# Optimization experiments

Measured on AMD Instinct MI355X. Metric: run time of the kernel, lower is better.

The kernel has to match this reference:

```python
import jax, jax.numpy as jnp
import numpy as np

NUM_LAYERS = 4
D_MODEL = 512
D_INNER = 1024   # 2 * d_model (Mamba expand=2)
D_STATE = 16
DT_RANK = 32     # ceil(d_model / 16)
D_CONV = 4
BATCH = 2
SEQ = 512
EPS = 1e-5


def _rmsnorm(x, w, eps=EPS):
    # fused add+RMSNorm math: fp32 reduction, scale by weight (no bias)
    x = x.astype(jnp.float32)
    return x * jax.lax.rsqrt(jnp.mean(x * x, axis=-1, keepdims=True) + eps) * w


def _silu(x):
    return x * jax.nn.sigmoid(x)


def _causal_conv(x, w, b):
    # x: (B, D, L); w: (D, K) depthwise causal conv, left-pad K-1, take first L
    xp = jnp.pad(x, ((0, 0), (0, 0), (D_CONV - 1, 0)))
    out = jax.lax.conv_general_dilated(
        xp, w[:, None, :], (1,), 'VALID',
        dimension_numbers=('NCH', 'OIH', 'NCH'),
        feature_group_count=x.shape[1])
    return out + b[None, :, None]


def _selective_scan(u, delta, A, Bm, Cm):
    # u, delta: (B, D, L); A: (D, N); Bm, Cm: (B, N, L)
    xs = (jnp.moveaxis(delta, 2, 0), jnp.moveaxis(u, 2, 0),
          jnp.moveaxis(Bm, 2, 0), jnp.moveaxis(Cm, 2, 0))
    h0 = jnp.zeros((u.shape[0], u.shape[1], A.shape[1]), u.dtype)

    def step(h, xst):
        d_t, u_t, b_t, c_t = xst                     # (B,D),(B,D),(B,N),(B,N)
        dA = jnp.exp(d_t[:, :, None] * A[None])      # (B,D,N) ZOH discretization
        h = h * dA + (d_t * u_t)[:, :, None] * b_t[:, None, :]
        y = jnp.einsum('bdn,bn->bd', h, c_t)
        return h, y

    _, ys = jax.lax.scan(step, h0, xs)
    return jnp.moveaxis(ys, 0, 2)                    # (B, D, L)


def _ssm_branch(x, z, cw, cb, xpw, dtw, dtb, Alog, Dskip):
    x = _silu(_causal_conv(x, cw, cb))                              # (B, Din, L)
    x_dbl = jnp.einsum('rd,bdl->brl', xpw, x)                       # (B, R+2N, L)
    dt, Bm, Cm = jnp.split(x_dbl, [DT_RANK, DT_RANK + D_STATE], axis=1)
    delta = jax.nn.softplus(jnp.einsum('dr,brl->bdl', dtw, dt) + dtb[None, :, None])
    A = -jnp.exp(Alog.astype(jnp.float32))                          # (Din, N)
    y = _selective_scan(x, delta, A, Bm, Cm)
    y = y + Dskip[None, :, None] * x
    return y * _silu(z)


def _encoder(x, norm_w, in_proj_w, convw_f, convb_f, xpw_f, dtw_f, dtb_f,
             Alog_f, Dskip_f, convw_r, convb_r, xpw_r, dtw_r, dtb_r,
             Alog_r, Dskip_r, out_proj_w, normf_w):
    residual = None
    hs = x
    feats = []
    for i in range(NUM_LAYERS):
        # fused add + RMSNorm, prenorm=True, residual_in_fp32
        residual = hs if residual is None else (hs + residual)
        residual = residual.astype(jnp.float32)
        hn = _rmsnorm(residual, norm_w[i])
        # bimamba v2 mixer
        xz = jnp.einsum('ed,bld->bel', in_proj_w[i], hn)            # (B, 2Din, L)
        xi, zi = jnp.split(xz, 2, axis=1)
        y_f = _ssm_branch(xi, zi, convw_f[i], convb_f[i], xpw_f[i], dtw_f[i],
                          dtb_f[i], Alog_f[i], Dskip_f[i])
        y_r = _ssm_branch(xi[:, :, ::-1], zi[:, :, ::-1], convw_r[i], convb_r[i],
                          xpw_r[i], dtw_r[i], dtb_r[i], Alog_r[i], Dskip_r[i])
        y = y_f + y_r[:, :, ::-1]
        hs = jnp.einsum('bel,de->bld', y, out_proj_w[i])
        feats.append(hs)
    out = _rmsnorm(hs + residual, normf_w)                          # prenorm=False
    return out, feats


def setup_inputs() -> dict:
    key = jax.random.key(0)
    ks = jax.random.split(key, 12)
    Ly = NUM_LAYERS
    s = 0.02

    def nrm(k, shape):
        return jax.random.normal(k, shape, jnp.float32) * s

    dt = 1e-3 + jax.random.uniform(ks[11], (Ly, D_INNER), jnp.float32) * (0.1 - 1e-3)
    dtb = jnp.log(jnp.expm1(dt))  # inverse softplus of dt init
    Alog = jnp.log(jnp.broadcast_to(
        jnp.arange(1, D_STATE + 1, dtype=jnp.float32), (Ly, D_INNER, D_STATE)))
    return dict(
        x=jax.random.normal(ks[0], (BATCH, SEQ, D_MODEL), jnp.float32),
        norm_w=jnp.ones((Ly, D_MODEL), jnp.float32),
        in_proj_w=nrm(ks[1], (Ly, 2 * D_INNER, D_MODEL)),
        convw_f=nrm(ks[2], (Ly, D_INNER, D_CONV)),
        convb_f=jnp.zeros((Ly, D_INNER), jnp.float32),
        xpw_f=nrm(ks[3], (Ly, DT_RANK + 2 * D_STATE, D_INNER)),
        dtw_f=nrm(ks[4], (Ly, D_INNER, DT_RANK)),
        dtb_f=dtb,
        Alog_f=Alog,
        Dskip_f=jnp.ones((Ly, D_INNER), jnp.float32),
        convw_r=nrm(ks[5], (Ly, D_INNER, D_CONV)),
        convb_r=jnp.zeros((Ly, D_INNER), jnp.float32),
        xpw_r=nrm(ks[6], (Ly, DT_RANK + 2 * D_STATE, D_INNER)),
        dtw_r=nrm(ks[7], (Ly, D_INNER, DT_RANK)),
        dtb_r=dtb,
        Alog_r=Alog,
        Dskip_r=jnp.ones((Ly, D_INNER), jnp.float32),
        out_proj_w=nrm(ks[8], (Ly, D_MODEL, D_INNER)),
        normf_w=jnp.ones((D_MODEL,), jnp.float32),
    )


def reference(x, norm_w, in_proj_w, convw_f, convb_f, xpw_f, dtw_f, dtb_f,
              Alog_f, Dskip_f, convw_r, convb_r, xpw_r, dtw_r, dtb_r,
              Alog_r, Dskip_r, out_proj_w, normf_w):
    out, feats = _encoder(x, norm_w, in_proj_w, convw_f, convb_f, xpw_f, dtw_f,
                          dtb_f, Alog_f, Dskip_f, convw_r, convb_r, xpw_r,
                          dtw_r, dtb_r, Alog_r, Dskip_r, out_proj_w, normf_w)
    return (out, jnp.stack(feats))
```

## Files before the change

### kernel.cpp

```cpp
#include <hip/hip_runtime.h>

#define BATCH 2
#define SEQ 512
#define DMODEL 512
#define DINNER 1024
#define DSTATE 16
#define DTRANK 32
#define NBL (BATCH*SEQ)
#define EPSV 1e-5f

typedef __attribute__((ext_vector_type(8))) short bf16x8;
typedef __attribute__((ext_vector_type(4))) float f32x4;

static __device__ __forceinline__ float sigmoidf_(float x) {
  return 1.0f / (1.0f + __expf(-x));
}
static __device__ __forceinline__ float softplusf_(float x) {
  return fmaxf(x, 0.0f) + log1pf(__expf(-fabsf(x)));
}
static __device__ __forceinline__ unsigned short f2bf(float x) {
  unsigned int u = __float_as_uint(x);
  unsigned int r = (u + 0x7FFFu + ((u >> 16) & 1u)) >> 16;
  return (unsigned short)r;
}

__global__ __launch_bounds__(256) void wconvert_kernel(
    const float* __restrict__ s0, const float* __restrict__ s1,
    const float* __restrict__ s2, const float* __restrict__ s3,
    const float* __restrict__ s4, const float* __restrict__ s5,
    unsigned short* __restrict__ d0, unsigned short* __restrict__ d1,
    unsigned short* __restrict__ d2, unsigned short* __restrict__ d3,
    unsigned short* __restrict__ d4, unsigned short* __restrict__ d5) {
  long i = (long)(blockIdx.x * 256 + threadIdx.x) * 8;
  const float* src; unsigned short* dst;
  if (i < 4194304)      { src = s0; dst = d0; }
  else if (i < 6291456) { src = s1; dst = d1; i -= 4194304; }
  else if (i < 6553600) { src = s2; dst = d2; i -= 6291456; }
  else if (i < 6815744) { src = s3; dst = d3; i -= 6553600; }
  else if (i < 6946816) { src = s4; dst = d4; i -= 6815744; }
  else                  { src = s5; dst = d5; i -= 6946816; }
  const float4 v0 = *(const float4*)&src[i];
  const float4 v1 = *(const float4*)&src[i + 4];
  bf16x8 o;
  o[0] = (short)f2bf(v0.x); o[1] = (short)f2bf(v0.y);
  o[2] = (short)f2bf(v0.z); o[3] = (short)f2bf(v0.w);
  o[4] = (short)f2bf(v1.x); o[5] = (short)f2bf(v1.y);
  o[6] = (short)f2bf(v1.z); o[7] = (short)f2bf(v1.w);
  *(bf16x8*)&dst[i] = o;
}

__global__ __launch_bounds__(256) void addnorm_kernel(
    const float* __restrict__ hs, float* __restrict__ residual,
    const float* __restrict__ w, float* __restrict__ out,
    unsigned short* __restrict__ outb, int first) {
  const int row = blockIdx.x;
  const int t = threadIdx.x;
  const float* hp = hs + (long)row * DMODEL;
  float* rp = residual + (long)row * DMODEL;
  float r0 = hp[t], r1 = hp[t + 256];
  if (!first) { r0 += rp[t]; r1 += rp[t + 256]; }
  rp[t] = r0; rp[t + 256] = r1;
  float ss = r0 * r0 + r1 * r1;
  #pragma unroll
  for (int off = 32; off; off >>= 1) ss += __shfl_xor(ss, off, 64);
  __shared__ float sw[4];
  const int wid = t >> 6, lane = t & 63;
  if (lane == 0) sw[wid] = ss;
  __syncthreads();
  const float tot = sw[0] + sw[1] + sw[2] + sw[3];
  const float scale = rsqrtf(tot * (1.0f / (float)DMODEL) + EPSV);
  const float v0 = r0 * scale * w[t];
  const float v1 = r1 * scale * w[t + 256];
  if (out) {
    out[(long)row * DMODEL + t] = v0;
    out[(long)row * DMODEL + t + 256] = v1;
  }
  if (outb) {
    outb[(long)row * DMODEL + t] = f2bf(v0);
    outb[(long)row * DMODEL + t + 256] = f2bf(v1);
  }
}

#define LDK 40
#define LDK2 72

__global__ __launch_bounds__(256) void gemm_in_kernel(
    const unsigned short* __restrict__ A, const unsigned short* __restrict__ B,
    float* __restrict__ C) {
  __shared__ unsigned short As[128 * LDK2];
  __shared__ unsigned short Bs[64 * LDK2];
  const int t = threadIdx.x;
  const int m0 = blockIdx.y * 128, n0 = blockIdx.x * 64;
  const int lane = t & 63;
  const int w = t >> 6;
  const int wr = (w >> 1) * 64, wc = (w & 1) * 32;
  const int fr = lane & 15;
  const int fq = lane >> 4;
  const int K = DMODEL;

  f32x4 acc[4][2];
  #pragma unroll
  for (int i = 0; i < 4; ++i)
    #pragma unroll
    for (int j = 0; j < 2; ++j) {
      f32x4 z = {0.f, 0.f, 0.f, 0.f};
      acc[i][j] = z;
    }

  const int arow = t >> 1, ako = (t & 1) * 32;
  const int brow = t >> 2, bko = (t & 3) * 16;

  bf16x8 pa[4], pb[2];
  #define LOADG_IN(k0_) do {                                              \
    const unsigned short* ap = &A[(long)(m0 + arow) * K + (k0_) + ako];   \
    pa[0] = *(const bf16x8*)ap;        pa[1] = *(const bf16x8*)(ap + 8);  \
    pa[2] = *(const bf16x8*)(ap + 16); pa[3] = *(const bf16x8*)(ap + 24); \
    const unsigned short* bp = &B[(long)(n0 + brow) * K + (k0_) + bko];   \
    pb[0] = *(const bf16x8*)bp;        pb[1] = *(const bf16x8*)(bp + 8);  \
  } while (0)

  LOADG_IN(0);
  for (int k0 = 0; k0 < K; k0 += 64) {
    if (k0) __syncthreads();
    *(bf16x8*)&As[arow * LDK2 + ako]      = pa[0];
    *(bf16x8*)&As[arow * LDK2 + ako + 8]  = pa[1];
    *(bf16x8*)&As[arow * LDK2 + ako + 16] = pa[2];
    *(bf16x8*)&As[arow * LDK2 + ako + 24] = pa[3];
    *(bf16x8*)&Bs[brow * LDK2 + bko]      = pb[0];
    *(bf16x8*)&Bs[brow * LDK2 + bko + 8]  = pb[1];
    __syncthreads();
    if (k0 + 64 < K) LOADG_IN(k0 + 64);
    #pragma unroll
    for (int h = 0; h < 2; ++h) {
      bf16x8 af[4], bg[2];
      #pragma unroll
      for (int i = 0; i < 4; ++i)
        af[i] = *(const bf16x8*)&As[(wr + i * 16 + fr) * LDK2 + h * 32 + fq * 8];
      #pragma unroll
      for (int j = 0; j < 2; ++j)
        bg[j] = *(const bf16x8*)&Bs[(wc + j * 16 + fr) * LDK2 + h * 32 + fq * 8];
      #pragma unroll
      for (int i = 0; i < 4; ++i)
        #pragma unroll
        for (int j = 0; j < 2; ++j)
          acc[i][j] = __builtin_amdgcn_mfma_f32_16x16x32_bf16(
              af[i], bg[j], acc[i][j], 0, 0, 0);
    }
  }
  #undef LOADG_IN

  #pragma unroll
  for (int i = 0; i < 4; ++i)
    #pragma unroll
    for (int j = 0; j < 2; ++j)
      #pragma unroll
      for (int r2 = 0; r2 < 4; ++r2) {
        const int m = m0 + wr + i * 16 + fq * 4 + r2;
        const int n = n0 + wc + j * 16 + fr;
        C[(long)m * NBL + n] = acc[i][j][r2];
      }
}

__global__ __launch_bounds__(256) void conv_silu_kernel(
    const float* __restrict__ xz,
    const float* __restrict__ cw_f, const float* __restrict__ cb_f,
    const float* __restrict__ cw_r, const float* __restrict__ cb_r,
    unsigned short* __restrict__ xcT) {
  __shared__ unsigned short tile[32][33];
  const int dir = blockIdx.z;
  const int n0 = blockIdx.x * 32, d0 = blockIdx.y * 32;
  const int b = n0 >> 9;
  const int l0 = n0 & (SEQ - 1);
  const float* cw = dir ? cw_r : cw_f;
  const float* cb = dir ? cb_r : cb_f;
  unsigned short* dst = xcT + (long)dir * DINNER * NBL;
  const int t = threadIdx.x;
  const int c = t & 31, rr = t >> 5;
  #pragma unroll
  for (int p = 0; p < 4; ++p) {
    const int d = d0 + p * 8 + rr;
    const int l = l0 + c;
    const float* xi = xz + (long)d * NBL + b * SEQ;
    float sum = cb[d];
    #pragma unroll
    for (int k = 0; k < 4; ++k) {
      const int tt = l - 3 + k;
      if (tt >= 0) {
        const int src = dir ? (SEQ - 1 - tt) : tt;
        sum += cw[d * 4 + k] * xi[src];
      }
    }
    const float v = sum * sigmoidf_(sum);
    tile[p * 8 + rr][c] = f2bf(v);
  }
  __syncthreads();
  #pragma unroll
  for (int p = 0; p < 4; ++p) {
    const int n = n0 + p * 8 + rr;
    dst[(long)n * DINNER + d0 + c] = tile[c][p * 8 + rr];
  }
}

__global__ __launch_bounds__(256) void xdbl_mfma_kernel(
    const unsigned short* __restrict__ xpwb_f, const unsigned short* __restrict__ xpwb_r,
    const unsigned short* __restrict__ xcT,
    unsigned short* __restrict__ dtT,
    float* __restrict__ xbc_f, float* __restrict__ xbc_r) {
  __shared__ unsigned short As[64 * LDK2];
  __shared__ unsigned short Bs[128 * LDK2];
  const int t = threadIdx.x;
  const int dir = blockIdx.y;
  const int n0 = blockIdx.x * 128;
  const unsigned short* A = dir ? xpwb_r : xpwb_f;
  const unsigned short* B = xcT + (long)dir * DINNER * NBL;
  float* xbc = dir ? xbc_r : xbc_f;
  unsigned short* dtt = dtT + (long)dir * NBL * DTRANK;

  const int lane = t & 63;
  const int w = t >> 6;
  const int fr = lane & 15;
  const int fq = lane >> 4;

  f32x4 acc[4][2];
  #pragma unroll
  for (int i = 0; i < 4; ++i)
    #pragma unroll
    for (int j = 0; j < 2; ++j) {
      f32x4 z = {0.f, 0.f, 0.f, 0.f};
      acc[i][j] = z;
    }

  const int arow = t >> 2, ako = (t & 3) * 16;
  const int brow = t >> 1, bko = (t & 1) * 32;

  bf16x8 pa[2], pb[4];
  #define LOADG_XD(k0_) do {                                                   \
    const unsigned short* ap = &A[(long)arow * DINNER + (k0_) + ako];          \
    pa[0] = *(const bf16x8*)ap;        pa[1] = *(const bf16x8*)(ap + 8);       \
    const unsigned short* bp = &B[(long)(n0 + brow) * DINNER + (k0_) + bko];   \
    pb[0] = *(const bf16x8*)bp;        pb[1] = *(const bf16x8*)(bp + 8);       \
    pb[2] = *(const bf16x8*)(bp + 16); pb[3] = *(const bf16x8*)(bp + 24);      \
  } while (0)

  LOADG_XD(0);
  for (int k0 = 0; k0 < DINNER; k0 += 64) {
    if (k0) __syncthreads();
    *(bf16x8*)&As[arow * LDK2 + ako]      = pa[0];
    *(bf16x8*)&As[arow * LDK2 + ako + 8]  = pa[1];
    *(bf16x8*)&Bs[brow * LDK2 + bko]      = pb[0];
    *(bf16x8*)&Bs[brow * LDK2 + bko + 8]  = pb[1];
    *(bf16x8*)&Bs[brow * LDK2 + bko + 16] = pb[2];
    *(bf16x8*)&Bs[brow * LDK2 + bko + 24] = pb[3];
    __syncthreads();
    if (k0 + 64 < DINNER) LOADG_XD(k0 + 64);
    #pragma unroll
    for (int h = 0; h < 2; ++h) {
      bf16x8 af[4], bg[2];
      #pragma unroll
      for (int i = 0; i < 4; ++i)
        af[i] = *(const bf16x8*)&As[(i * 16 + fr) * LDK2 + h * 32 + fq * 8];
      #pragma unroll
      for (int j = 0; j < 2; ++j)
        bg[j] = *(const bf16x8*)&Bs[(w * 32 + j * 16 + fr) * LDK2 + h * 32 + fq * 8];
      #pragma unroll
      for (int i = 0; i < 4; ++i)
        #pragma unroll
        for (int j = 0; j < 2; ++j)
          acc[i][j] = __builtin_amdgcn_mfma_f32_16x16x32_bf16(
              af[i], bg[j], acc[i][j], 0, 0, 0);
    }
  }
  #undef LOADG_XD

  #pragma unroll
  for (int i = 0; i < 4; ++i)
    #pragma unroll
    for (int j = 0; j < 2; ++j)
      #pragma unroll
      for (int r2 = 0; r2 < 4; ++r2) {
        const int m = i * 16 + fq * 4 + r2;
        const int n = n0 + w * 32 + j * 16 + fr;
        const float v = acc[i][j][r2];
        if (m < DTRANK) dtt[(long)n * DTRANK + m] = f2bf(v);
        else xbc[(long)(m - 32) * NBL + n] = v;
      }
}

__global__ __launch_bounds__(256) void deltam_kernel(
    const unsigned short* __restrict__ dtwb_f, const unsigned short* __restrict__ dtwb_r,
    const unsigned short* __restrict__ dtT,
    const float* __restrict__ dtb_f, const float* __restrict__ dtb_r,
    float* __restrict__ delta_f, float* __restrict__ delta_r) {
  __shared__ unsigned short As[128 * LDK];
  __shared__ unsigned short Bs[128 * LDK];
  const int t = threadIdx.x;
  const int dir = blockIdx.z;
  const unsigned short* A = dir ? dtwb_r : dtwb_f;
  const unsigned short* B = dtT + (long)dir * NBL * DTRANK;
  const float* dtb = dir ? dtb_r : dtb_f;
  float* dl = dir ? delta_r : delta_f;
  const int m0 = blockIdx.y * 128, n0 = blockIdx.x * 128;
  const int lane = t & 63;
  const int w = t >> 6;
  const int wr = (w >> 1) * 64, wc = (w & 1) * 64;
  const int fr = lane & 15;
  const int fq = lane >> 4;

  const int srow = t >> 1;
  const int sko = (t & 1) * 16;
  *(bf16x8*)&As[srow * LDK + sko] =
      *(const bf16x8*)&A[(long)(m0 + srow) * DTRANK + sko];
  *(bf16x8*)&As[srow * LDK + sko + 8] =
      *(const bf16x8*)&A[(long)(m0 + srow) * DTRANK + sko + 8];
  *(bf16x8*)&Bs[srow * LDK + sko] =
      *(const bf16x8*)&B[(long)(n0 + srow) * DTRANK + sko];
  *(bf16x8*)&Bs[srow * LDK + sko + 8] =
      *(const bf16x8*)&B[(long)(n0 + srow) * DTRANK + sko + 8];
  __syncthreads();

  bf16x8 af[4], bg[4];
  #pragma unroll
  for (int i = 0; i < 4; ++i) {
    af[i] = *(const bf16x8*)&As[(wr + i * 16 + fr) * LDK + fq * 8];
    bg[i] = *(const bf16x8*)&Bs[(wc + i * 16 + fr) * LDK + fq * 8];
  }
  f32x4 acc[4][4];
  #pragma unroll
  for (int i = 0; i < 4; ++i)
    #pragma unroll
    for (int j = 0; j < 4; ++j) {
      f32x4 z = {0.f, 0.f, 0.f, 0.f};
      acc[i][j] = __builtin_amdgcn_mfma_f32_16x16x32_bf16(af[i], bg[j], z, 0, 0, 0);
    }

  #pragma unroll
  for (int i = 0; i < 4; ++i) {
    const int m = m0 + wr + i * 16 + fq * 4;
    #pragma unroll
    for (int r2 = 0; r2 < 4; ++r2) {
      const float bias = dtb[m + r2];
      #pragma unroll
      for (int j = 0; j < 4; ++j) {
        const int n = n0 + wc + j * 16 + fr;
        dl[(long)(m + r2) * NBL + n] = softplusf_(acc[i][j][r2] + bias);
      }
    }
  }
}

static __device__ __forceinline__ void scan_pass(
    const float* __restrict__ dp, const float u[8],
    const float* __restrict__ bct, const float* __restrict__ Alog,
    float Dv, int lane, float out[8]) {
  float dt[8], dtu[8];
  {
    const float4 a0 = *(const float4*)&dp[0];
    const float4 a1 = *(const float4*)&dp[4];
    dt[0] = a0.x; dt[1] = a0.y; dt[2] = a0.z; dt[3] = a0.w;
    dt[4] = a1.x; dt[5] = a1.y; dt[6] = a1.z; dt[7] = a1.w;
  }
  #pragma unroll
  for (int j = 0; j < 8; ++j) { dtu[j] = dt[j] * u[j]; out[j] = 0.f; }

  for (int n = 0; n < DSTATE; ++n) {
    const float An = -__expf(Alog[n]);
    float Bv[8], Cv[8], dA[8], cB[8];
    {
      const float* bp = bct + (long)n * NBL;
      const float* cp = bct + (long)(DSTATE + n) * NBL;
      const float4 b0 = *(const float4*)&bp[0];
      const float4 b1 = *(const float4*)&bp[4];
      Bv[0] = b0.x; Bv[1] = b0.y; Bv[2] = b0.z; Bv[3] = b0.w;
      Bv[4] = b1.x; Bv[5] = b1.y; Bv[6] = b1.z; Bv[7] = b1.w;
      const float4 c0 = *(const float4*)&cp[0];
      const float4 c1 = *(const float4*)&cp[4];
      Cv[0] = c0.x; Cv[1] = c0.y; Cv[2] = c0.z; Cv[3] = c0.w;
      Cv[4] = c1.x; Cv[5] = c1.y; Cv[6] = c1.z; Cv[7] = c1.w;
    }
    float h = 0.f, P = 1.f;
    #pragma unroll
    for (int j = 0; j < 8; ++j) {
      dA[j] = __expf(dt[j] * An);
      cB[j] = dtu[j] * Bv[j];
      h = fmaf(h, dA[j], cB[j]);
      P *= dA[j];
    }
    float hs = h, Ps = P;
    #pragma unroll
    for (int off = 1; off < 64; off <<= 1) {
      const float hp = __shfl_up(hs, off, 64);
      const float Pp = __shfl_up(Ps, off, 64);
      if (lane >= off) { hs = fmaf(hp, Ps, hs); Ps *= Pp; }
    }
    float h0 = __shfl_up(hs, 1, 64);
    if (lane == 0) h0 = 0.f;
    #pragma unroll
    for (int j = 0; j < 8; ++j) {
      h0 = fmaf(h0, dA[j], cB[j]);
      out[j] = fmaf(h0, Cv[j], out[j]);
    }
  }
  #pragma unroll
  for (int j = 0; j < 8; ++j) out[j] = fmaf(Dv, u[j], out[j]);
}

__global__ __launch_bounds__(256) void scan_merged_kernel(
    const float* __restrict__ delta_f, const float* __restrict__ delta_r,
    const float* __restrict__ xbc_f, const float* __restrict__ xbc_r,
    const float* __restrict__ Alog_f, const float* __restrict__ Alog_r,
    const float* __restrict__ Dsk_f, const float* __restrict__ Dsk_r,
    const float* __restrict__ cw_f, const float* __restrict__ cb_f,
    const float* __restrict__ cw_r, const float* __restrict__ cb_r,
    const float* __restrict__ xz, unsigned short* __restrict__ ybt) {
  __shared__ unsigned short s_t[4][512];
  const int t = threadIdx.x;
  const int wv = t >> 6;
  const int lane = t & 63;
  const int row = blockIdx.x * 4 + wv;
  const int b = row >> 10, d = row & 1023;
  const long rbase = (long)d * NBL + b * SEQ;

  float xv[8];
  {
    const float* xp = xz + rbase + lane * 8;
    const float4 a0 = *(const float4*)&xp[0];
    const float4 a1 = *(const float4*)&xp[4];
    xv[0] = a0.x; xv[1] = a0.y; xv[2] = a0.z; xv[3] = a0.w;
    xv[4] = a1.x; xv[5] = a1.y; xv[6] = a1.z; xv[7] = a1.w;
  }
  float uf[8];
  {
    float cw0 = cw_f[d * 4], cw1 = cw_f[d * 4 + 1], cw2 = cw_f[d * 4 + 2],
          cw3 = cw_f[d * 4 + 3], cb = cb_f[d];
    float xm1 = __shfl_up(xv[7], 1, 64);
    float xm2 = __shfl_up(xv[6], 1, 64);
    float xm3 = __shfl_up(xv[5], 1, 64);
    const float ext[3] = {xm3, xm2, xm1};
    #pragma unroll
    for (int j = 0; j < 8; ++j) {
      float s = cb + cw3 * xv[j];
      const int p = lane * 8 + j;
      #pragma unroll
      for (int k = 0; k < 3; ++k) {
        const int idx = j - 3 + k;
        const float xval = (idx >= 0) ? xv[idx] : ext[3 + idx];
        if (p - 3 + k >= 0) s += (k == 0 ? cw0 : (k == 1 ? cw1 : cw2)) * xval;
      }
      uf[j] = s * sigmoidf_(s);
    }
  }
  float xr[8];
  #pragma unroll
  for (int j = 0; j < 8; ++j) xr[j] = __shfl(xv[7 - j], 63 - lane, 64);
  float ur[8];
  {
    float cw0 = cw_r[d * 4], cw1 = cw_r[d * 4 + 1], cw2 = cw_r[d * 4 + 2],
          cw3 = cw_r[d * 4 + 3], cb = cb_r[d];
    float xm1 = __shfl_up(xr[7], 1, 64);
    float xm2 = __shfl_up(xr[6], 1, 64);
    float xm3 = __shfl_up(xr[5], 1, 64);
    const float ext[3] = {xm3, xm2, xm1};
    #pragma unroll
    for (int j = 0; j < 8; ++j) {
      float s = cb + cw3 * xr[j];
      const int p = lane * 8 + j;
      #pragma unroll
      for (int k = 0; k < 3; ++k) {
        const int idx = j - 3 + k;
        const float xval = (idx >= 0) ? xr[idx] : ext[3 + idx];
        if (p - 3 + k >= 0) s += (k == 0 ? cw0 : (k == 1 ? cw1 : cw2)) * xval;
      }
      ur[j] = s * sigmoidf_(s);
    }
  }

  float af[8], ar[8];
  scan_pass(delta_f + rbase + lane * 8, uf,
            xbc_f + b * SEQ + lane * 8, Alog_f + d * DSTATE, Dsk_f[d], lane, af);
  scan_pass(delta_r + rbase + lane * 8, ur,
            xbc_r + b * SEQ + lane * 8, Alog_r + d * DSTATE, Dsk_r[d], lane, ar);

  const float* zp = xz + (long)(DINNER + d) * NBL + b * SEQ + lane * 8;
  const float4 z0 = *(const float4*)&zp[0];
  const float4 z1 = *(const float4*)&zp[4];
  const float zv[8] = {z0.x, z0.y, z0.z, z0.w, z1.x, z1.y, z1.z, z1.w};
  bf16x8 obf;
  #pragma unroll
  for (int j = 0; j < 8; ++j) {
    const float v = __shfl(ar[7 - j], 63 - lane, 64);
    obf[j] = (short)f2bf((af[j] + v) * (zv[j] * sigmoidf_(zv[j])));
  }
  *(bf16x8*)&s_t[wv][lane * 8] = obf;
  __syncthreads();
  const int d0 = (blockIdx.x * 4) & 1023;
  const int bb = (blockIdx.x * 4) >> 10;
  unsigned short* yrow = ybt + (long)(bb * SEQ) * DINNER + d0;
  #pragma unroll
  for (int q = 0; q < 2; ++q) {
    const int n = t * 2 + q;
    ushort4 v = {s_t[0][n], s_t[1][n], s_t[2][n], s_t[3][n]};
    *(ushort4*)&yrow[(long)n * DINNER] = v;
  }
}

__global__ __launch_bounds__(256) void gemm_out_kernel(
    const unsigned short* __restrict__ A, const unsigned short* __restrict__ B,
    float* __restrict__ C) {
  __shared__ unsigned short As[128 * LDK2];
  __shared__ unsigned short Bs[128 * LDK2];
  const int t = threadIdx.x;
  const int m0 = blockIdx.y * 128, n0 = blockIdx.x * 128;
  const int lane = t & 63;
  const int w = t >> 6;
  const int wr = (w >> 1) * 64, wc = (w & 1) * 64;
  const int fr = lane & 15;
  const int fq = lane >> 4;
  const int K = DINNER;

  f32x4 acc[4][4];
  #pragma unroll
  for (int i = 0; i < 4; ++i)
    #pragma unroll
    for (int j = 0; j < 4; ++j) {
      f32x4 z = {0.f, 0.f, 0.f, 0.f};
      acc[i][j] = z;
    }

  const int srow = t >> 1, sko = (t & 1) * 32;

  bf16x8 pa[4], pb[4];
  #define LOADG_OUT(k0_) do {                                              \
    const unsigned short* ap = &A[(long)(m0 + srow) * K + (k0_) + sko];    \
    pa[0] = *(const bf16x8*)ap;        pa[1] = *(const bf16x8*)(ap + 8);   \
    pa[2] = *(const bf16x8*)(ap + 16); pa[3] = *(const bf16x8*)(ap + 24);  \
    const unsigned short* bp = &B[(long)(n0 + srow) * K + (k0_) + sko];    \
    pb[0] = *(const bf16x8*)bp;        pb[1] = *(const bf16x8*)(bp + 8);   \
    pb[2] = *(const bf16x8*)(bp + 16); pb[3] = *(const bf16x8*)(bp + 24);  \
  } while (0)

  LOADG_OUT(0);
  for (int k0 = 0; k0 < K; k0 += 64) {
    if (k0) __syncthreads();
    *(bf16x8*)&As[srow * LDK2 + sko]      = pa[0];
    *(bf16x8*)&As[srow * LDK2 + sko + 8]  = pa[1];
    *(bf16x8*)&As[srow * LDK2 + sko + 16] = pa[2];
    *(bf16x8*)&As[srow * LDK2 + sko + 24] = pa[3];
    *(bf16x8*)&Bs[srow * LDK2 + sko]      = pb[0];
    *(bf16x8*)&Bs[srow * LDK2 + sko + 8]  = pb[1];
    *(bf16x8*)&Bs[srow * LDK2 + sko + 16] = pb[2];
    *(bf16x8*)&Bs[srow * LDK2 + sko + 24] = pb[3];
    __syncthreads();
    if (k0 + 64 < K) LOADG_OUT(k0 + 64);
    #pragma unroll
    for (int h = 0; h < 2; ++h) {
      bf16x8 af[4], bg[4];
      #pragma unroll
      for (int i = 0; i < 4; ++i) {
        af[i] = *(const bf16x8*)&As[(wr + i * 16 + fr) * LDK2 + h * 32 + fq * 8];
        bg[i] = *(const bf16x8*)&Bs[(wc + i * 16 + fr) * LDK2 + h * 32 + fq * 8];
      }
      #pragma unroll
      for (int i = 0; i < 4; ++i)
        #pragma unroll
        for (int j = 0; j < 4; ++j)
          acc[i][j] = __builtin_amdgcn_mfma_f32_16x16x32_bf16(
              af[i], bg[j], acc[i][j], 0, 0, 0);
    }
  }
  #undef LOADG_OUT

  #pragma unroll
  for (int i = 0; i < 4; ++i)
    #pragma unroll
    for (int j = 0; j < 4; ++j)
      #pragma unroll
      for (int r2 = 0; r2 < 4; ++r2) {
        const int m = m0 + wr + i * 16 + fq * 4 + r2;
        const int n = n0 + wc + j * 16 + fr;
        C[(long)n * DMODEL + m] = acc[i][j][r2];
      }
}

extern "C" void kernel_launch(void* const* d_in, const int* in_sizes, int n_in,
                              void* d_out, int out_size, void* d_ws, size_t ws_size,
                              hipStream_t stream) {
  (void)in_sizes; (void)n_in; (void)out_size; (void)ws_size;
  const float* x       = (const float*)d_in[0];
  const float* norm_w  = (const float*)d_in[1];
  const float* in_proj = (const float*)d_in[2];
  const float* convw_f = (const float*)d_in[3];
  const float* convb_f = (const float*)d_in[4];
  const float* xpw_f   = (const float*)d_in[5];
  const float* dtw_f   = (const float*)d_in[6];
  const float* dtb_f   = (const float*)d_in[7];
  const float* Alog_f  = (const float*)d_in[8];
  const float* Dsk_f   = (const float*)d_in[9];
  const float* convw_r = (const float*)d_in[10];
  const float* convb_r = (const float*)d_in[11];
  const float* xpw_r   = (const float*)d_in[12];
  const float* dtw_r   = (const float*)d_in[13];
  const float* dtb_r   = (const float*)d_in[14];
  const float* Alog_r  = (const float*)d_in[15];
  const float* Dsk_r   = (const float*)d_in[16];
  const float* out_w   = (const float*)d_in[17];
  const float* normf_w = (const float*)d_in[18];

  float* ws = (float*)d_ws;
  float* residual = ws;  ws += 524288;
  float* xzbuf    = ws;  ws += 2097152;
  float* xbc_f    = ws;  ws += 32768;
  float* xbc_r    = ws;  ws += 32768;
  float* delta_f  = ws;  ws += 1048576;
  float* delta_r  = ws;  ws += 1048576;
  float* hnb_f    = ws;  ws += 262144;
  float* wbfin_f  = ws;  ws += 2097152;
  float* wbfout_f = ws;  ws += 1048576;
  float* ybt_f    = ws;  ws += 524288;
  float* xcT_f    = ws;  ws += 1048576;
  float* dtT_f    = ws;  ws += 32768;
  float* xpwb_f_  = ws;  ws += 131072;
  float* xpwb_r_  = ws;  ws += 131072;
  float* dtwb_f_  = ws;  ws += 65536;
  float* dtwb_r_  = ws;  ws += 65536;

  unsigned short* hnb = (unsigned short*)hnb_f;
  unsigned short* wbfin = (unsigned short*)wbfin_f;
  unsigned short* wbfout = (unsigned short*)wbfout_f;
  unsigned short* ybt = (unsigned short*)ybt_f;
  unsigned short* xcT = (unsigned short*)xcT_f;
  unsigned short* dtT = (unsigned short*)dtT_f;
  unsigned short* xpwb_f = (unsigned short*)xpwb_f_;
  unsigned short* xpwb_r = (unsigned short*)xpwb_r_;
  unsigned short* dtwb_f = (unsigned short*)dtwb_f_;
  unsigned short* dtwb_r = (unsigned short*)dtwb_r_;

  float* outp = (float*)d_out;

  wconvert_kernel<<<3456, 256, 0, stream>>>(
      in_proj, out_w, xpw_f, xpw_r, dtw_f, dtw_r,
      wbfin, wbfout, xpwb_f, xpwb_r, dtwb_f, dtwb_r);

  for (int layer = 0; layer < 4; ++layer) {
    const float* hsrc = layer == 0 ? x : (outp + (long)layer * 524288);
    addnorm_kernel<<<1024, 256, 0, stream>>>(
        hsrc, residual, norm_w + layer * DMODEL, nullptr, hnb, layer == 0 ? 1 : 0);
    gemm_in_kernel<<<dim3(16, 16), 256, 0, stream>>>(
        wbfin + (long)layer * 2048 * 512, hnb, xzbuf);
    conv_silu_kernel<<<dim3(32, 32, 2), 256, 0, stream>>>(
        xzbuf, convw_f + layer * DINNER * 4, convb_f + layer * DINNER,
        convw_r + layer * DINNER * 4, convb_r + layer * DINNER, xcT);
    xdbl_mfma_kernel<<<dim3(8, 2), 256, 0, stream>>>(
        xpwb_f + (long)layer * 64 * DINNER, xpwb_r + (long)layer * 64 * DINNER,
        xcT, dtT, xbc_f, xbc_r);
    deltam_kernel<<<dim3(8, 8, 2), 256, 0, stream>>>(
        dtwb_f + (long)layer * DINNER * DTRANK, dtwb_r + (long)layer * DINNER * DTRANK,
        dtT, dtb_f + layer * DINNER, dtb_r + layer * DINNER, delta_f, delta_r);
    scan_merged_kernel<<<512, 256, 0, stream>>>(
        delta_f, delta_r, xbc_f, xbc_r,
        Alog_f + layer * DINNER * DSTATE, Alog_r + layer * DINNER * DSTATE,
        Dsk_f + layer * DINNER, Dsk_r + layer * DINNER,
        convw_f + layer * DINNER * 4, convb_f + layer * DINNER,
        convw_r + layer * DINNER * 4, convb_r + layer * DINNER,
        xzbuf, ybt);
    gemm_out_kernel<<<dim3(8, 4), 256, 0, stream>>>(
        wbfout + (long)layer * 512 * 1024, ybt,
        outp + (long)(1 + layer) * 524288);
  }
  addnorm_kernel<<<1024, 256, 0, stream>>>(
      outp + 4 * 524288, residual, normf_w, outp, nullptr, 0);
}
```

Baseline: 389.9 us.

## Split forward and reverse scan directions across separate wavefronts

The merged scan kernel ran both the forward and the reverse selective scan one after the other in a single wavefront. Each direction now gets its own wavefront in a 512-thread block, and the reverse result is exchanged through shared memory before the forward wave applies the gate and writes bf16 output. This doubles wave-level parallelism for the latency-bound scan. In exchange it adds an extra barrier and shared-memory traffic, and each direction reloads x.

```diff
diff --git a/kernel.cpp b/kernel.cpp
--- a/kernel.cpp
+++ b/kernel.cpp
@@ -404,7 +404,7 @@
   for (int j = 0; j < 8; ++j) out[j] = fmaf(Dv, u[j], out[j]);
 }
 
-__global__ __launch_bounds__(256) void scan_merged_kernel(
+__global__ __launch_bounds__(512) void scan_split_kernel(
     const float* __restrict__ delta_f, const float* __restrict__ delta_r,
     const float* __restrict__ xbc_f, const float* __restrict__ xbc_r,
     const float* __restrict__ Alog_f, const float* __restrict__ Alog_r,
@@ -412,11 +412,14 @@
     const float* __restrict__ cw_f, const float* __restrict__ cb_f,
     const float* __restrict__ cw_r, const float* __restrict__ cb_r,
     const float* __restrict__ xz, unsigned short* __restrict__ ybt) {
-  __shared__ unsigned short s_t[4][512];
+  __shared__ float s_r[4][512];
+  __shared__ unsigned short s_y[4][512];
   const int t = threadIdx.x;
   const int wv = t >> 6;
   const int lane = t & 63;
-  const int row = blockIdx.x * 4 + wv;
+  const int dir = wv & 1;
+  const int dl = wv >> 1;
+  const int row = blockIdx.x * 4 + dl;
   const int b = row >> 10, d = row & 1023;
   const long rbase = (long)d * NBL + b * SEQ;
 
@@ -428,13 +431,22 @@
     xv[0] = a0.x; xv[1] = a0.y; xv[2] = a0.z; xv[3] = a0.w;
     xv[4] = a1.x; xv[5] = a1.y; xv[6] = a1.z; xv[7] = a1.w;
   }
-  float uf[8];
+  if (dir) {
+    float xr[8];
+    #pragma unroll
+    for (int j = 0; j < 8; ++j) xr[j] = __shfl(xv[7 - j], 63 - lane, 64);
+    #pragma unroll
+    for (int j = 0; j < 8; ++j) xv[j] = xr[j];
+  }
+  const float* cwp = dir ? cw_r : cw_f;
+  const float* cbp = dir ? cb_r : cb_f;
+  float u[8];
   {
-    float cw0 = cw_f[d * 4], cw1 = cw_f[d * 4 + 1], cw2 = cw_f[d * 4 + 2],
-          cw3 = cw_f[d * 4 + 3], cb = cb_f[d];
-    float xm1 = __shfl_up(xv[7], 1, 64);
-    float xm2 = __shfl_up(xv[6], 1, 64);
-    float xm3 = __shfl_up(xv[5], 1, 64);
+    const float cw0 = cwp[d * 4], cw1 = cwp[d * 4 + 1], cw2 = cwp[d * 4 + 2],
+                cw3 = cwp[d * 4 + 3], cb = cbp[d];
+    const float xm1 = __shfl_up(xv[7], 1, 64);
+    const float xm2 = __shfl_up(xv[6], 1, 64);
+    const float xm3 = __shfl_up(xv[5], 1, 64);
     const float ext[3] = {xm3, xm2, xm1};
     #pragma unroll
     for (int j = 0; j < 8; ++j) {
@@ -446,59 +458,42 @@
         const float xval = (idx >= 0) ? xv[idx] : ext[3 + idx];
         if (p - 3 + k >= 0) s += (k == 0 ? cw0 : (k == 1 ? cw1 : cw2)) * xval;
       }
-      uf[j] = s * sigmoidf_(s);
-    }
-  }
-  float xr[8];
-  #pragma unroll
-  for (int j = 0; j < 8; ++j) xr[j] = __shfl(xv[7 - j], 63 - lane, 64);
-  float ur[8];
-  {
-    float cw0 = cw_r[d * 4], cw1 = cw_r[d * 4 + 1], cw2 = cw_r[d * 4 + 2],
-          cw3 = cw_r[d * 4 + 3], cb = cb_r[d];
-    float xm1 = __shfl_up(xr[7], 1, 64);
-    float xm2 = __shfl_up(xr[6], 1, 64);
-    float xm3 = __shfl_up(xr[5], 1, 64);
-    const float ext[3] = {xm3, xm2, xm1};
+      u[j] = s * sigmoidf_(s);
+    }
+  }
+
+  float a[8];
+  scan_pass((dir ? delta_r : delta_f) + rbase + lane * 8, u,
+            (dir ? xbc_r : xbc_f) + b * SEQ + lane * 8,
+            (dir ? Alog_r : Alog_f) + d * DSTATE,
+            (dir ? Dsk_r : Dsk_f)[d], lane, a);
+
+  if (dir) {
     #pragma unroll
     for (int j = 0; j < 8; ++j) {
-      float s = cb + cw3 * xr[j];
-      const int p = lane * 8 + j;
-      #pragma unroll
-      for (int k = 0; k < 3; ++k) {
-        const int idx = j - 3 + k;
-        const float xval = (idx >= 0) ? xr[idx] : ext[3 + idx];
-        if (p - 3 + k >= 0) s += (k == 0 ? cw0 : (k == 1 ? cw1 : cw2)) * xval;
-      }
-      ur[j] = s * sigmoidf_(s);
-    }
-  }
-
-  float af[8], ar[8];
-  scan_pass(delta_f + rbase + lane * 8, uf,
-            xbc_f + b * SEQ + lane * 8, Alog_f + d * DSTATE, Dsk_f[d], lane, af);
-  scan_pass(delta_r + rbase + lane * 8, ur,
-            xbc_r + b * SEQ + lane * 8, Alog_r + d * DSTATE, Dsk_r[d], lane, ar);
-
-  const float* zp = xz + (long)(DINNER + d) * NBL + b * SEQ + lane * 8;
-  const float4 z0 = *(const float4*)&zp[0];
-  const float4 z1 = *(const float4*)&zp[4];
-  const float zv[8] = {z0.x, z0.y, z0.z, z0.w, z1.x, z1.y, z1.z, z1.w};
-  bf16x8 obf;
-  #pragma unroll
-  for (int j = 0; j < 8; ++j) {
-    const float v = __shfl(ar[7 - j], 63 - lane, 64);
-    obf[j] = (short)f2bf((af[j] + v) * (zv[j] * sigmoidf_(zv[j])));
-  }
-  *(bf16x8*)&s_t[wv][lane * 8] = obf;
+      const float v = __shfl(a[7 - j], 63 - lane, 64);
+      s_r[dl][lane * 8 + j] = v;
+    }
+  }
+  __syncthreads();
+  if (!dir) {
+    const float* zp = xz + (long)(DINNER + d) * NBL + b * SEQ + lane * 8;
+    const float4 z0 = *(const float4*)&zp[0];
+    const float4 z1 = *(const float4*)&zp[4];
+    const float zv[8] = {z0.x, z0.y, z0.z, z0.w, z1.x, z1.y, z1.z, z1.w};
+    #pragma unroll
+    for (int j = 0; j < 8; ++j) {
+      const float tot = a[j] + s_r[dl][lane * 8 + j];
+      s_y[dl][lane * 8 + j] = f2bf(tot * (zv[j] * sigmoidf_(zv[j])));
+    }
+  }
   __syncthreads();
   const int d0 = (blockIdx.x * 4) & 1023;
   const int bb = (blockIdx.x * 4) >> 10;
   unsigned short* yrow = ybt + (long)(bb * SEQ) * DINNER + d0;
-  #pragma unroll
-  for (int q = 0; q < 2; ++q) {
-    const int n = t * 2 + q;
-    ushort4 v = {s_t[0][n], s_t[1][n], s_t[2][n], s_t[3][n]};
+  {
+    const int n = t;
+    ushort4 v = {s_y[0][n], s_y[1][n], s_y[2][n], s_y[3][n]};
     *(ushort4*)&yrow[(long)n * DINNER] = v;
   }
 }
@@ -655,7 +650,7 @@
     deltam_kernel<<<dim3(8, 8, 2), 256, 0, stream>>>(
         dtwb_f + (long)layer * DINNER * DTRANK, dtwb_r + (long)layer * DINNER * DTRANK,
         dtT, dtb_f + layer * DINNER, dtb_r + layer * DINNER, delta_f, delta_r);
-    scan_merged_kernel<<<512, 256, 0, stream>>>(
+    scan_split_kernel<<<512, 512, 0, stream>>>(
         delta_f, delta_r, xbc_f, xbc_r,
         Alog_f + layer * DINNER * DSTATE, Alog_r + layer * DINNER * DSTATE,
         Dsk_f + layer * DINNER, Dsk_r + layer * DINNER,
```

New measurement: 366.7 us. 1.06x faster.
